# Kernel optimization log

Measured on AMD Instinct MI355X. Metric: run time of the kernel, lower is better.

## Reference

```python
import jax, jax.numpy as jnp
import numpy as np

B, C, H, W = 4, 64, 256, 256
HEADS = 4
HID = 128  # dim * ffn_expansion_factor
EPS = 1e-5


def _ln_chan(x, w, b):
    # LayerNorm over channel axis of [b,c,h,w] (equiv to to_3d -> LN over c -> to_4d)
    mu = x.mean(1, keepdims=True)
    var = jnp.mean((x - mu) ** 2, axis=1, keepdims=True)
    return (x - mu) / jnp.sqrt(var + EPS) * w[None, :, None, None] + b[None, :, None, None]


def _ln_last(x, w, b):
    mu = x.mean(-1, keepdims=True)
    var = jnp.mean((x - mu) ** 2, axis=-1, keepdims=True)
    return (x - mu) / jnp.sqrt(var + EPS) * w + b


def _conv1(x, Wt):
    # 1x1 conv, no bias; Wt: [out,in]
    return jnp.einsum('oi,bihw->bohw', Wt, x)


def _l2norm(x):
    # torch F.normalize(dim=-1): x / max(||x||, 1e-12)
    return x / jnp.maximum(jnp.linalg.norm(x, axis=-1, keepdims=True), 1e-12)


def _dct(inp1, inp2, Wq, Wk, Wv, temp):
    # Divide_Cross_Transformer: q from inp2, k/v from inp1; channel-wise attention
    b, c, h, w = inp1.shape
    ch = c // HEADS
    hw = h * w
    q = _conv1(inp2, Wq).reshape(b, HEADS, ch, hw)
    k = _conv1(inp1, Wk).reshape(b, HEADS, ch, hw)
    v = _conv1(inp1, Wv).reshape(b, HEADS, ch, hw)
    q = _l2norm(q)
    k = _l2norm(k)
    attn = jax.nn.softmax(jnp.einsum('bhcn,bhdn->bhcd', q, k) * temp[None], axis=-1)
    return attn, v  # attn: [b,head,ch,ch], v: [b,head,ch,hw]


def _ffn(x3, w1, b1, w2, b2):
    # torch nn.GELU default = exact erf
    hdn = jax.nn.gelu(jnp.einsum('bnc,hc->bnh', x3, w1) + b1, approximate=False)
    return jnp.einsum('bnh,ch->bnc', hdn, w2) + b2


def setup_inputs() -> dict:
    key = jax.random.key(0)
    ks = jax.random.split(key, 16)
    s = 0.05

    def n(k, shape):
        return jax.random.normal(k, shape, jnp.float32) * s

    ones = jnp.ones((C,), jnp.float32)
    zeros = jnp.zeros((C,), jnp.float32)
    return {
        'image': jax.random.normal(ks[0], (B, C, H, W), jnp.float32),
        'event': jax.random.normal(ks[1], (B, C, H, W), jnp.float32),
        'Wq_c': n(ks[2], (C, C)), 'Wk_c': n(ks[3], (C, C)), 'Wv_c': n(ks[4], (C, C)),
        'temp_c': jnp.ones((HEADS, 1, 1), jnp.float32),
        'Wq_d': n(ks[5], (C, C)), 'Wk_d': n(ks[6], (C, C)), 'Wv_d': n(ks[7], (C, C)),
        'temp_d': jnp.ones((HEADS, 1, 1), jnp.float32),
        'ln_img_w': ones, 'ln_img_b': zeros,
        'ln_evt_w': ones, 'ln_evt_b': zeros,
        'ln_com_w': ones, 'ln_com_b': zeros,
        'ln_dif_w': ones, 'ln_dif_b': zeros,
        'ln1_w': ones, 'ln1_b': zeros,
        'ln2_w': ones, 'ln2_b': zeros,
        'fc1c_w': n(ks[8], (HID, C)), 'fc1c_b': jnp.zeros((HID,), jnp.float32),
        'fc2c_w': n(ks[9], (C, HID)), 'fc2c_b': jnp.zeros((C,), jnp.float32),
        'fc1d_w': n(ks[10], (HID, C)), 'fc1d_b': jnp.zeros((HID,), jnp.float32),
        'fc2d_w': n(ks[11], (C, HID)), 'fc2d_b': jnp.zeros((C,), jnp.float32),
        'proj1_w': n(ks[12], (C, C)), 'proj2_w': n(ks[13], (C, C)),
    }


def reference(image, event, Wq_c, Wk_c, Wv_c, temp_c, Wq_d, Wk_d, Wv_d, temp_d,
              ln_img_w, ln_img_b, ln_evt_w, ln_evt_b, ln_com_w, ln_com_b,
              ln_dif_w, ln_dif_b, ln1_w, ln1_b, ln2_w, ln2_b,
              fc1c_w, fc1c_b, fc2c_w, fc2c_b, fc1d_w, fc1d_b, fc2d_w, fc2d_b,
              proj1_w, proj2_w):
    b, c, h, w = image.shape
    hw = h * w
    common = image + event
    differential = image - event

    ni = _ln_chan(image, ln_img_w, ln_img_b)
    ne = _ln_chan(event, ln_evt_w, ln_evt_b)
    nc = _ln_chan(common, ln_com_w, ln_com_b)
    nd = _ln_chan(differential, ln_dif_w, ln_dif_b)

    # common branch: shared conv weights (attn_common), attn maps multiplied
    a_ic, v_ic = _dct(ni, nc, Wq_c, Wk_c, Wv_c, temp_c)
    a_ec, v_ec = _dct(ne, nc, Wq_c, Wk_c, Wv_c, temp_c)
    a_c = a_ic * a_ec
    oc = jnp.einsum('bhcd,bhdn->bhcn', a_c, v_ic + v_ec)  # same attn for both matmuls
    oc = oc.reshape(b, c, h, w)
    oc = _conv1(oc, proj1_w)
    oc3 = oc.reshape(b, c, hw).transpose(0, 2, 1)  # b (hw) c
    oc3 = oc3 + _ffn(_ln_last(oc3, ln1_w, ln1_b), fc1c_w, fc1c_b, fc2c_w, fc2c_b)
    out_common = oc3.transpose(0, 2, 1).reshape(b, c, h, w)

    # differential branch: separate attn maps, not multiplied
    a_id, v_id = _dct(ni, nd, Wq_d, Wk_d, Wv_d, temp_d)
    a_ed, v_ed = _dct(ne, nd, Wq_d, Wk_d, Wv_d, temp_d)
    od = (jnp.einsum('bhcd,bhdn->bhcn', a_id, v_id)
          + jnp.einsum('bhcd,bhdn->bhcn', a_ed, v_ed))
    od = od.reshape(b, c, h, w)
    od = _conv1(od, proj2_w)
    od3 = od.reshape(b, c, hw).transpose(0, 2, 1)
    od3 = od3 + _ffn(_ln_last(od3, ln2_w, ln2_b), fc1d_w, fc1d_b, fc2d_w, fc2d_b)
    out_differential = od3.transpose(0, 2, 1).reshape(b, c, h, w)

    return (out_common, out_differential)
```

## Files before the change

kernel.cpp:

```cpp
#include <hip/hip_runtime.h>
#include <math.h>

typedef unsigned int u32;
typedef unsigned short u16;
typedef __attribute__((ext_vector_type(8))) short short8;
typedef __attribute__((ext_vector_type(4))) float float4v;

#define NBATCH 4
#define HW 65536

#define OFF_COV 0
#define OFF_T   131072
#define OFF_M   294912
#define OFF_P   344064
#define OFF_WC  393216
#define OFF_PAR 516096
#define WS_NEED ((size_t)(OFF_PAR + 1048576) * 4)

__device__ inline float bf2f(u16 h){ return __uint_as_float(((u32)h) << 16); }
__device__ inline u16 f2bf(float x){
  u32 u = __float_as_uint(x);
  u += 0x7fffu + ((u >> 16) & 1u);
  return (u16)(u >> 16);
}
__device__ inline u32 packbf2(float a, float b){
  u32 r;
  asm("v_cvt_pk_bf16_f32 %0, %1, %2" : "=v"(r) : "v"(a), "v"(b));
  return r;
}
__device__ inline float bfu(u32 u, int hi){
  return __uint_as_float(hi ? (u & 0xffff0000u) : (u << 16));
}

__device__ inline bool detect_f32(const void* probe, int t, int* s_cnt){
  if (t == 0) *s_cnt = 0;
  __syncthreads();
  u32 w = ((const u32*)probe)[t & 255];
  u32 ex = (w >> 7) & 0xffu;
  if (!(ex >= 113u && ex <= 133u)) atomicAdd(s_cnt, 1);
  __syncthreads();
  return *s_cnt >= 128;
}

__device__ inline bool detect_f32_512(const void* probe, int t, int* s_cnt){
  if (t == 0) *s_cnt = 0;
  __syncthreads();
  if (t < 256){
    u32 w = ((const u32*)probe)[t];
    u32 ex = (w >> 7) & 0xffu;
    if (!(ex >= 113u && ex <= 133u)) atomicAdd(s_cnt, 1);
  }
  __syncthreads();
  return *s_cnt >= 128;
}

__device__ inline void ld8(const u16* pb, const float* pf, size_t idx, bool f32, float* o){
  if (f32){
    const float4 a = *(const float4*)(pf + idx);
    const float4 b = *(const float4*)(pf + idx + 4);
    o[0]=a.x; o[1]=a.y; o[2]=a.z; o[3]=a.w; o[4]=b.x; o[5]=b.y; o[6]=b.z; o[7]=b.w;
  } else {
    uint4 r = *(const uint4*)(pb + idx);
    const u32* p = (const u32*)&r;
    #pragma unroll
    for (int j=0;j<8;j++) o[j] = bfu(p[j>>1], j&1);
  }
}

__device__ inline void softmax16(float* l){
  float m = l[0];
  #pragma unroll
  for (int i=1;i<16;i++) m = fmaxf(m, l[i]);
  float s = 0.f;
  #pragma unroll
  for (int i=0;i<16;i++){ l[i] = __expf(l[i]-m); s += l[i]; }
  float r = 1.0f/s;
  #pragma unroll
  for (int i=0;i<16;i++) l[i] *= r;
}

__global__ __launch_bounds__(256) void convert_all(
    const void* img,
    const void* t0, const void* t1, const void* t2, const void* t3,
    const void* t4, const void* t5, const void* t6, const void* t7,
    const void* t8, const void* t9, const void* t10, const void* t11,
    const void* t12, const void* t13, const void* t14, const void* t15,
    const void* t16, const void* t17, const void* t18, const void* t19,
    const void* t20, const void* t21, const void* t22, const void* t23,
    const void* t24, const void* t25, const void* t26, const void* t27,
    const void* t28, const void* t29,
    u16* __restrict__ wc)
{
  __shared__ int s_cnt;
  const int t = threadIdx.x;
  const bool f32 = detect_f32(img, t, &s_cnt);
  const int sizes[30] = {4096,4096,4096,4,4096,4096,4096,4,
                         64,64,64,64,64,64,64,64,64,64,64,64,
                         8192,128,8192,64,8192,128,8192,64,4096,4096};
  const void* srcs[30] = {t0,t1,t2,t3,t4,t5,t6,t7,t8,t9,t10,t11,t12,t13,t14,
                          t15,t16,t17,t18,t19,t20,t21,t22,t23,t24,t25,t26,t27,t28,t29};
  const int id = blockIdx.x;
  const void* s = srcs[id];
  const int n = sizes[id];
  u16* d = wc + (size_t)id*8192;
  for (int j = t; j < n; j += 256)
    d[j] = f32 ? f2bf(((const float*)s)[j]) : ((const u16*)s)[j];
}

__global__ __launch_bounds__(512, 4) void k1_cov(
    const void* __restrict__ img, const void* __restrict__ evt,
    const u16* __restrict__ lniw, const u16* __restrict__ lnib,
    const u16* __restrict__ lnew, const u16* __restrict__ lneb,
    const u16* __restrict__ lncw, const u16* __restrict__ lncb,
    const u16* __restrict__ lndw, const u16* __restrict__ lndb,
    float* __restrict__ cov, float* __restrict__ par, int use_par)
{
  __shared__ u16 NtL[4*64*72];
  __shared__ float spart[8][64][5];
  __shared__ float params[8][64];
  __shared__ int s_cnt;

  const int t = threadIdx.x;
  const bool f32 = detect_f32_512(img, t, &s_cnt);
  const u16* imgb = (const u16*)img; const float* imgf = (const float*)img;
  const u16* evtb = (const u16*)evt; const float* evtf = (const float*)evt;

  const int b = blockIdx.x >> 7;
  const int P0 = (blockIdx.x & 127) * 512;
  const int ch = t >> 3, pg = t & 7;
  const int wave = t >> 6, lane = t & 63, l15 = lane & 15, quad = lane >> 4;

  float wi=bf2f(lniw[ch]), bi=bf2f(lnib[ch]);
  float we=bf2f(lnew[ch]), be=bf2f(lneb[ch]);
  float wc_=bf2f(lncw[ch]), bc_=bf2f(lncb[ch]);
  float wd_=bf2f(lndw[ch]), bd_=bf2f(lndb[ch]);

  const int va = (wave==3)?0 : (wave==7)?1 : (wave<3)?2:3;
  const int vb = (wave==0)?2 : (wave==4)?3 :
                 ((wave==2)||(wave==6)||(wave==7))?1:0;

  float4v acc[4][4];
  #pragma unroll
  for (int i=0;i<4;i++)
    #pragma unroll
    for (int j=0;j<4;j++) acc[i][j]=(float4v)0.f;

  const size_t base = (size_t)(b*64 + ch) * HW;

  for (int it = 0; it < 8; ++it){
    const int p0 = P0 + it*64;
    float A[8], B[8];
    ld8(imgb, imgf, base + p0 + pg*8, f32, A);
    ld8(evtb, evtf, base + p0 + pg*8, f32, B);

    #pragma unroll 1
    for (int jp=0;jp<4;jp++){
// ... 233 lines not shown

__global__ __launch_bounds__(256) void p2c(
    const u16* __restrict__ proj1, const u16* __restrict__ proj2,
    float* __restrict__ ws)
{
  __shared__ float WL[64][65];
  __shared__ float CL[64][64];
  const int t = threadIdx.x;
  const int b = blockIdx.x & 3;
  const int which = blockIdx.x >> 2;
  const u16* W = (which==0)? proj1 : proj2;
  const float* Cm = ws + OFF_M + ((size_t)which*NBATCH + b)*4096;
  { int r = t>>2, c0 = (t&3)*16;
    #pragma unroll
    for (int i=0;i<16;i++) WL[r][c0+i] = bf2f(W[r*64 + c0 + i]);
    const float4* s = (const float4*)(Cm + r*64 + c0);
    float4* d = (float4*)&CL[r][c0];
    d[0]=s[0]; d[1]=s[1]; d[2]=s[2]; d[3]=s[3]; }
  __syncthreads();
  const int r = t>>2, k0 = (t&3)*16;
  float a[16];
  #pragma unroll
  for (int i=0;i<16;i++) a[i]=0.f;
  for (int m=0;m<64;m++){
    float wv = WL[r][m];
    #pragma unroll
    for (int i=0;i<16;i++) a[i] = fmaf(wv, CL[m][k0+i], a[i]);
  }
  float* o = ws + OFF_P + ((size_t)which*NBATCH + b)*4096 + r*64 + k0;
  #pragma unroll
  for (int i=0;i<16;i++) o[i] = a[i];
}

__global__ __launch_bounds__(256) void k3_common(
    const void* __restrict__ img, const void* __restrict__ evt,
    const u16* __restrict__ lniw, const u16* __restrict__ lnib,
    const u16* __restrict__ lnew, const u16* __restrict__ lneb,
    const u16* __restrict__ ln1w, const u16* __restrict__ ln1b,
    const u16* __restrict__ fc1w, const u16* __restrict__ fc1b,
    const u16* __restrict__ fc2w, const u16* __restrict__ fc2b,
    const float* __restrict__ Pmat, void* __restrict__ outp, size_t obase,
    const float* __restrict__ par, int use_par)
{
  __shared__ u16 fc1L[128*72];
  __shared__ u16 fc2L[64*136];
  __shared__ u16 PcL[64*72];
  __shared__ u16 SB[64*136];
  __shared__ float spart[4][64][4];
  __shared__ float params[64][4];
  __shared__ float b1L[128];
  __shared__ float b2L[64];
  __shared__ int s_cnt;

  const int t = threadIdx.x;
  const bool f32 = detect_f32(img, t, &s_cnt);
  const u16* imgb = (const u16*)img; const float* imgf = (const float*)img;
  const u16* evtb = (const u16*)evt; const float* evtf = (const float*)evt;

  const int b = blockIdx.x >> 8;
  const int P0 = (blockIdx.x & 255) * 256;
  const int chg = t >> 3, pg = t & 7, ch0 = chg*2;
  const int wave = t >> 6, lane = t & 63, l15 = lane & 15, quad = lane >> 4;

  { int row = t >> 1, c0 = (t & 1)*32;
    const uint4* s = (const uint4*)(fc1w + row*64 + c0);
    uint4* d = (uint4*)&fc1L[row*72 + c0];
    d[0]=s[0]; d[1]=s[1]; d[2]=s[2]; d[3]=s[3]; }
  { int row = t >> 2, c0 = (t & 3)*32;
    const uint4* s = (const uint4*)(fc2w + row*128 + c0);
    uint4* d = (uint4*)&fc2L[row*136 + c0];
    d[0]=s[0]; d[1]=s[1]; d[2]=s[2]; d[3]=s[3]; }
  { int row = t >> 2, c0 = (t & 3)*16;
    const float* s = Pmat + (size_t)b*4096 + row*64 + c0;
    u32 u[8];
    #pragma unroll
    for (int i=0;i<8;i++) u[i] = packbf2(s[2*i], s[2*i+1]);
    uint4* d = (uint4*)&PcL[row*72 + c0];
    d[0] = make_uint4(u[0],u[1],u[2],u[3]);
    d[1] = make_uint4(u[4],u[5],u[6],u[7]); }
  if (t < 128) b1L[t] = bf2f(fc1b[t]);
  if (t < 64)  b2L[t] = bf2f(fc2b[t]);

  float wi0=bf2f(lniw[ch0]), wi1=bf2f(lniw[ch0+1]);
  float we0=bf2f(lnew[ch0]), we1=bf2f(lnew[ch0+1]);
  float bs0=bf2f(lnib[ch0]) + bf2f(lneb[ch0]);
  float bs1=bf2f(lnib[ch0+1]) + bf2f(lneb[ch0+1]);
  float w1r[4], b1r[4];
  #pragma unroll
  for (int nj=0;nj<4;nj++){ w1r[nj]=bf2f(ln1w[nj*16+l15]); b1r[nj]=bf2f(ln1b[nj*16+l15]); }
  __syncthreads();

  const size_t base_i = (size_t)(b*64 + ch0)*HW;
  for (int it=0; it<4; ++it){
    const int p0 = P0 + it*64;
    float A0[8], A1[8], B0[8], B1[8];
    ld8(imgb, imgf, base_i + p0 + pg*8, f32, A0);
    ld8(imgb, imgf, base_i + HW + p0 + pg*8, f32, A1);
    ld8(evtb, evtf, base_i + p0 + pg*8, f32, B0);
    ld8(evtb, evtf, base_i + HW + p0 + pg*8, f32, B1);

    if (use_par){
      const float4* pp = (const float4*)(par + ((size_t)b*HW + p0 + pg*8)*4);
      #pragma unroll
      for (int j=0;j<8;j++){
        float4 pr = pp[j];
        float a0=(A0[j]-pr.x)*pr.y, a1=(A1[j]-pr.x)*pr.y;
        float c0f=(B0[j]-pr.z)*pr.w, c1f=(B1[j]-pr.z)*pr.w;
        float n0 = fmaf(a0, wi0, fmaf(c0f, we0, bs0));
        float n1 = fmaf(a1, wi1, fmaf(c1f, we1, bs1));
        *(u32*)&SB[(pg*8+j)*136 + ch0] = packbf2(n0, n1);
      }
    } else {
      float si[8], sii[8], se[8], see[8];
      #pragma unroll
      for (int j=0;j<8;j++){
        float xi0=A0[j], xi1=A1[j], xe0=B0[j], xe1=B1[j];
        si[j]=xi0+xi1; sii[j]=fmaf(xi0,xi0,xi1*xi1);
        se[j]=xe0+xe1; see[j]=fmaf(xe0,xe0,xe1*xe1);
      }
      #pragma unroll
      for (int m=8;m<=32;m<<=1)
        #pragma unroll
        for (int j=0;j<8;j++){
          si[j]+=__shfl_xor(si[j],m); sii[j]+=__shfl_xor(sii[j],m);
          se[j]+=__shfl_xor(se[j],m); see[j]+=__shfl_xor(see[j],m);
        }
      if ((chg&7)==0){
        #pragma unroll
        for (int j=0;j<8;j++){
          spart[wave][pg*8+j][0]=si[j]; spart[wave][pg*8+j][1]=sii[j];
          spart[wave][pg*8+j][2]=se[j]; spart[wave][pg*8+j][3]=see[j];
        }
      }
      __syncthreads();
      if (t<64){
        float S0=0,S1=0,S2=0,S3=0;
        #pragma unroll
        for (int w=0;w<4;w++){ S0+=spart[w][t][0]; S1+=spart[w][t][1]; S2+=spart[w][t][2]; S3+=spart[w][t][3]; }
        const float inv=0.015625f;
        float mu_i=S0*inv, mu_e=S2*inv;
        float r_i=rsqrtf(fmaf(S1,inv,-mu_i*mu_i)+1e-5f);
        float r_e=rsqrtf(fmaf(S3,inv,-mu_e*mu_e)+1e-5f);
        params[t][0]=mu_i; params[t][1]=r_i; params[t][2]=mu_e; params[t][3]=r_e;
      }
      __syncthreads();
      #pragma unroll
      for (int j=0;j<8;j++){
        float4 pr = *(const float4*)&params[pg*8+j][0];
        float a0=(A0[j]-pr.x)*pr.y, a1=(A1[j]-pr.x)*pr.y;
        float c0f=(B0[j]-pr.z)*pr.w, c1f=(B1[j]-pr.z)*pr.w;
        float n0 = fmaf(a0, wi0, fmaf(c0f, we0, bs0));
        float n1 = fmaf(a1, wi1, fmaf(c1f, we1, bs1));
        *(u32*)&SB[(pg*8+j)*136 + ch0] = packbf2(n0, n1);
      }
    }
    __syncthreads();
    float4v acc1[4];
    #pragma unroll
    for (int nj=0;nj<4;nj++) acc1[nj]=(float4v)0.f;
    const int px_row = wave*16 + l15;
    #pragma unroll
    for (int ks=0;ks<2;ks++){
      const int off = ks*32 + quad*8;
      short8 af = *(const short8*)&SB[px_row*136 + off];
      #pragma unroll
      for (int nj=0;nj<4;nj++){
        short8 bw = *(const short8*)&PcL[(nj*16+l15)*72 + off];
        acc1[nj] = __builtin_amdgcn_mfma_f32_16x16x32_bf16(af, bw, acc1[nj], 0,0,0);
      }
    }
    float s[4], sq[4];
    #pragma unroll
    for (int j=0;j<4;j++){
      s[j] = acc1[0][j]+acc1[1][j]+acc1[2][j]+acc1[3][j];
      sq[j] = acc1[0][j]*acc1[0][j];
      sq[j] = fmaf(acc1[1][j],acc1[1][j],sq[j]);
      sq[j] = fmaf(acc1[2][j],acc1[2][j],sq[j]);
      sq[j] = fmaf(acc1[3][j],acc1[3][j],sq[j]);
    }
    #pragma unroll
    for (int m=1;m<=8;m<<=1)
      #pragma unroll
      for (int j=0;j<4;j++){ s[j]+=__shfl_xor(s[j],m); sq[j]+=__shfl_xor(sq[j],m); }
    float muj[4], rj[4];
    #pragma unroll
    for (int j=0;j<4;j++){
      muj[j]=s[j]*0.015625f;
// ... 31 lines not shown
      }
    }
    float4v accO[4];
    #pragma unroll
    for (int nj=0;nj<4;nj++) accO[nj]=(float4v)0.f;
    #pragma unroll
    for (int ks=0;ks<4;ks++){
      const int off = ks*32+quad*8;
      short8 ag = *(const short8*)&SB[px_row*136 + off];
      #pragma unroll
      for (int nj=0;nj<4;nj++){
        short8 bw = *(const short8*)&fc2L[(nj*16+l15)*136 + off];
        accO[nj] = __builtin_amdgcn_mfma_f32_16x16x32_bf16(ag, bw, accO[nj], 0,0,0);
      }
    }
    const int px0 = p0 + wave*16 + quad*4;
    #pragma unroll
    for (int nj=0;nj<4;nj++){
      float bb = b2L[nj*16+l15];
      int r = nj*16+l15;
      float v0 = acc1[nj][0] + accO[nj][0] + bb;
      float v1 = acc1[nj][1] + accO[nj][1] + bb;
      float v2 = acc1[nj][2] + accO[nj][2] + bb;
      float v3 = acc1[nj][3] + accO[nj][3] + bb;
      size_t oi = obase + (size_t)(b*64 + r)*HW + px0;
      if (f32){ float4 fv; fv.x=v0; fv.y=v1; fv.z=v2; fv.w=v3;
        *(float4*)((float*)outp + oi) = fv; }
      else *(uint2*)((u16*)outp + oi) = make_uint2(packbf2(v0,v1), packbf2(v2,v3));
    }
    __syncthreads();
  }
}

__global__ __launch_bounds__(256) void k3_diff(
    const void* __restrict__ img, const void* __restrict__ evt,
    const u16* __restrict__ lniw, const u16* __restrict__ lnib,
    const u16* __restrict__ lnew, const u16* __restrict__ lneb,
    const u16* __restrict__ ln2w, const u16* __restrict__ ln2b,
    const u16* __restrict__ fc1w, const u16* __restrict__ fc1b,
    const u16* __restrict__ fc2w, const u16* __restrict__ fc2b,
    const float* __restrict__ Pmat, void* __restrict__ outp, size_t obase,
    const float* __restrict__ par, int use_par)
{
  __shared__ u16 fc1L[128*72];
  __shared__ u16 fc2L[64*136];
  __shared__ u16 PiL[64*72];
  __shared__ u16 PeL[64*72];
  __shared__ u16 N2L[64*144];
  __shared__ float spart[4][64][4];
  __shared__ float params[64][4];
  __shared__ float b1L[128];
  __shared__ float b2L[64];
  __shared__ int s_cnt;

  const int t = threadIdx.x;
  const bool f32 = detect_f32(img, t, &s_cnt);
  const u16* imgb = (const u16*)img; const float* imgf = (const float*)img;
  const u16* evtb = (const u16*)evt; const float* evtf = (const float*)evt;

  const int b = blockIdx.x >> 8;
  const int P0 = (blockIdx.x & 255) * 256;
  const int chg = t >> 3, pg = t & 7, ch0 = chg*2;
  const int wave = t >> 6, lane = t & 63, l15 = lane & 15, quad = lane >> 4;

  { int row = t >> 1, c0 = (t & 1)*32;
    const uint4* s = (const uint4*)(fc1w + row*64 + c0);
    uint4* d = (uint4*)&fc1L[row*72 + c0];
    d[0]=s[0]; d[1]=s[1]; d[2]=s[2]; d[3]=s[3]; }
  { int row = t >> 2, c0 = (t & 3)*32;
    const uint4* s = (const uint4*)(fc2w + row*128 + c0);
    uint4* d = (uint4*)&fc2L[row*136 + c0];
    d[0]=s[0]; d[1]=s[1]; d[2]=s[2]; d[3]=s[3]; }
  { int row = t >> 2, c0 = (t & 3)*16;
    const float* si_ = Pmat + ((size_t)1*NBATCH + b)*4096 + row*64 + c0;
    const float* se_ = Pmat + ((size_t)2*NBATCH + b)*4096 + row*64 + c0;
    u32 u[8];
    #pragma unroll
    for (int i=0;i<8;i++) u[i] = packbf2(si_[2*i], si_[2*i+1]);
    uint4* d = (uint4*)&PiL[row*72 + c0];
    d[0] = make_uint4(u[0],u[1],u[2],u[3]); d[1] = make_uint4(u[4],u[5],u[6],u[7]);
    #pragma unroll
    for (int i=0;i<8;i++) u[i] = packbf2(se_[2*i], se_[2*i+1]);
    uint4* d2 = (uint4*)&PeL[row*72 + c0];
    d2[0] = make_uint4(u[0],u[1],u[2],u[3]); d2[1] = make_uint4(u[4],u[5],u[6],u[7]); }
  if (t < 128) b1L[t] = bf2f(fc1b[t]);
  if (t < 64)  b2L[t] = bf2f(fc2b[t]);

  float wi0=bf2f(lniw[ch0]), wi1=bf2f(lniw[ch0+1]);
  float bi0=bf2f(lnib[ch0]), bi1=bf2f(lnib[ch0+1]);
  float we0=bf2f(lnew[ch0]), we1=bf2f(lnew[ch0+1]);
  float be0=bf2f(lneb[ch0]), be1=bf2f(lneb[ch0+1]);
  float w1r[4], b1r[4];
  #pragma unroll
  for (int nj=0;nj<4;nj++){ w1r[nj]=bf2f(ln2w[nj*16+l15]); b1r[nj]=bf2f(ln2b[nj*16+l15]); }
  __syncthreads();

  const size_t base_i = (size_t)(b*64 + ch0)*HW;
  for (int it=0; it<4; ++it){
    const int p0 = P0 + it*64;
    float A0[8], A1[8], B0[8], B1[8];
    ld8(imgb, imgf, base_i + p0 + pg*8, f32, A0);
    ld8(imgb, imgf, base_i + HW + p0 + pg*8, f32, A1);
    ld8(evtb, evtf, base_i + p0 + pg*8, f32, B0);
    ld8(evtb, evtf, base_i + HW + p0 + pg*8, f32, B1);

    if (use_par){
      const float4* pp = (const float4*)(par + ((size_t)b*HW + p0 + pg*8)*4);
      #pragma unroll
      for (int j=0;j<8;j++){
        float4 pr = pp[j];
        float a0=(A0[j]-pr.x)*pr.y, a1=(A1[j]-pr.x)*pr.y;
        float c0f=(B0[j]-pr.z)*pr.w, c1f=(B1[j]-pr.z)*pr.w;
        *(u32*)&N2L[(pg*8+j)*144 + ch0]      = packbf2(fmaf(a0,wi0,bi0), fmaf(a1,wi1,bi1));
        *(u32*)&N2L[(pg*8+j)*144 + 72 + ch0] = packbf2(fmaf(c0f,we0,be0), fmaf(c1f,we1,be1));
      }
    } else {
      float si[8], sii[8], se[8], see[8];
      #pragma unroll
      for (int j=0;j<8;j++){
        float xi0=A0[j], xi1=A1[j], xe0=B0[j], xe1=B1[j];
        si[j]=xi0+xi1; sii[j]=fmaf(xi0,xi0,xi1*xi1);
        se[j]=xe0+xe1; see[j]=fmaf(xe0,xe0,xe1*xe1);
      }
      #pragma unroll
      for (int m=8;m<=32;m<<=1)
        #pragma unroll
        for (int j=0;j<8;j++){
          si[j]+=__shfl_xor(si[j],m); sii[j]+=__shfl_xor(sii[j],m);
          se[j]+=__shfl_xor(se[j],m); see[j]+=__shfl_xor(see[j],m);
        }
      if ((chg&7)==0){
        #pragma unroll
        for (int j=0;j<8;j++){
          spart[wave][pg*8+j][0]=si[j]; spart[wave][pg*8+j][1]=sii[j];
          spart[wave][pg*8+j][2]=se[j]; spart[wave][pg*8+j][3]=see[j];
        }
      }
      __syncthreads();
      if (t<64){
        float S0=0,S1=0,S2=0,S3=0;
        #pragma unroll
        for (int w=0;w<4;w++){ S0+=spart[w][t][0]; S1+=spart[w][t][1]; S2+=spart[w][t][2]; S3+=spart[w][t][3]; }
        const float inv=0.015625f;
        float mu_i=S0*inv, mu_e=S2*inv;
        float r_i=rsqrtf(fmaf(S1,inv,-mu_i*mu_i)+1e-5f);
        float r_e=rsqrtf(fmaf(S3,inv,-mu_e*mu_e)+1e-5f);
        params[t][0]=mu_i; params[t][1]=r_i; params[t][2]=mu_e; params[t][3]=r_e;
      }
      __syncthreads();
      #pragma unroll
      for (int j=0;j<8;j++){
        float4 pr = *(const float4*)&params[pg*8+j][0];
        float a0=(A0[j]-pr.x)*pr.y, a1=(A1[j]-pr.x)*pr.y;
        float c0f=(B0[j]-pr.z)*pr.w, c1f=(B1[j]-pr.z)*pr.w;
        *(u32*)&N2L[(pg*8+j)*144 + ch0]      = packbf2(fmaf(a0,wi0,bi0), fmaf(a1,wi1,bi1));
        *(u32*)&N2L[(pg*8+j)*144 + 72 + ch0] = packbf2(fmaf(c0f,we0,be0), fmaf(c1f,we1,be1));
      }
    }
    __syncthreads();
    float4v acc1[4];
    #pragma unroll
    for (int nj=0;nj<4;nj++) acc1[nj]=(float4v)0.f;
    const int px_row = wave*16 + l15;
    #pragma unroll
    for (int ks=0;ks<2;ks++){
      const int off = ks*32 + quad*8;
      short8 ai = *(const short8*)&N2L[px_row*144 + off];
      short8 ae = *(const short8*)&N2L[px_row*144 + 72 + off];
      #pragma unroll
      for (int nj=0;nj<4;nj++){
        short8 bwi = *(const short8*)&PiL[(nj*16+l15)*72 + off];
        acc1[nj] = __builtin_amdgcn_mfma_f32_16x16x32_bf16(ai, bwi, acc1[nj], 0,0,0);
        short8 bwe = *(const short8*)&PeL[(nj*16+l15)*72 + off];
        acc1[nj] = __builtin_amdgcn_mfma_f32_16x16x32_bf16(ae, bwe, acc1[nj], 0,0,0);
      }
    }
    float s[4], sq[4];
    #pragma unroll
    for (int j=0;j<4;j++){
      s[j] = acc1[0][j]+acc1[1][j]+acc1[2][j]+acc1[3][j];
      sq[j] = acc1[0][j]*acc1[0][j];
      sq[j] = fmaf(acc1[1][j],acc1[1][j],sq[j]);
      sq[j] = fmaf(acc1[2][j],acc1[2][j],sq[j]);
      sq[j] = fmaf(acc1[3][j],acc1[3][j],sq[j]);
    }
    #pragma unroll
    for (int m=1;m<=8;m<<=1)
      #pragma unroll
      for (int j=0;j<4;j++){ s[j]+=__shfl_xor(s[j],m); sq[j]+=__shfl_xor(sq[j],m); }
    float muj[4], rj[4];
// ... 59 lines not shown
      if (f32){ float4 fv; fv.x=v0; fv.y=v1; fv.z=v2; fv.w=v3;
        *(float4*)((float*)outp + oi) = fv; }
      else *(uint2*)((u16*)outp + oi) = make_uint2(packbf2(v0,v1), packbf2(v2,v3));
    }
    __syncthreads();
  }
}

extern "C" void kernel_launch(void* const* d_in, const int* in_sizes, int n_in,
                              void* d_out, int out_size, void* d_ws, size_t ws_size,
                              hipStream_t stream)
{
  const void* img = d_in[0];
  const void* evt = d_in[1];
  float* ws = (float*)d_ws;
  u16* wc = (u16*)(ws + OFF_WC);
  float* par = ws + OFF_PAR;
  const int use_par = (ws_size >= WS_NEED) ? 1 : 0;
  #define SLOT(i) (wc + (size_t)((i)-2)*8192)

  hipMemsetAsync(ws, 0, 131072*sizeof(float), stream);
  convert_all<<<dim3(30), dim3(256), 0, stream>>>(img,
      d_in[2], d_in[3], d_in[4], d_in[5], d_in[6], d_in[7], d_in[8], d_in[9],
      d_in[10], d_in[11], d_in[12], d_in[13], d_in[14], d_in[15], d_in[16], d_in[17],
      d_in[18], d_in[19], d_in[20], d_in[21], d_in[22], d_in[23], d_in[24], d_in[25],
      d_in[26], d_in[27], d_in[28], d_in[29], d_in[30], d_in[31], wc);
  k1_cov<<<dim3(512), dim3(512), 0, stream>>>(img, evt,
      SLOT(10), SLOT(11), SLOT(12), SLOT(13), SLOT(14), SLOT(15), SLOT(16), SLOT(17),
      ws, par, use_par);
  p2a<<<dim3(40), dim3(256), 0, stream>>>(SLOT(2), SLOT(3), SLOT(6), SLOT(7), ws);
  p2b<<<dim3(4), dim3(256), 0, stream>>>(ws, SLOT(2), SLOT(3), SLOT(6), SLOT(7),
      SLOT(4), SLOT(8), SLOT(5), SLOT(9));
  p2c<<<dim3(12), dim3(256), 0, stream>>>(SLOT(30), SLOT(31), ws);
  k3_common<<<dim3(1024), dim3(256), 0, stream>>>(img, evt,
      SLOT(10), SLOT(11), SLOT(12), SLOT(13), SLOT(18), SLOT(19),
      SLOT(22), SLOT(23), SLOT(24), SLOT(25), ws + OFF_P, d_out, (size_t)0, par, use_par);
  k3_diff<<<dim3(1024), dim3(256), 0, stream>>>(img, evt,
      SLOT(10), SLOT(11), SLOT(12), SLOT(13), SLOT(20), SLOT(21),
      SLOT(26), SLOT(27), SLOT(28), SLOT(29), ws + OFF_P, d_out, (size_t)16777216, par, use_par);
  #undef SLOT
}
```

Measured before the change: 567.9 us.

## Add larger-block k3 kernels specialized for precomputed LayerNorm params

Adds k3_common_hi (512 threads, 512 pixels per block) and k3_diff_hi (1024 threads, 1024 pixels per block) that always read the precomputed per-pixel LN parameters. They are dispatched when the workspace is large enough, and the original kernels keep only the in-kernel statistics path. The aim is to spread the weight and projection staging into LDS over more pixels per block and to remove the runtime branch. The cost is much larger LDS per block, especially the 256x144 buffer in the diff kernel, which can lower occupancy. Unused ld8_issue/ld8_unpack helpers are also added.

```diff
diff --git a/kernel.cpp b/kernel.cpp
--- a/kernel.cpp
+++ b/kernel.cpp
@@ -42,7 +42,7 @@
   return *s_cnt >= 128;
 }
 
-__device__ inline bool detect_f32_512(const void* probe, int t, int* s_cnt){
+__device__ inline bool detect_f32_wide(const void* probe, int t, int* s_cnt){
   if (t == 0) *s_cnt = 0;
   __syncthreads();
   if (t < 256){
@@ -62,6 +62,26 @@
   } else {
     uint4 r = *(const uint4*)(pb + idx);
     const u32* p = (const u32*)&r;
+    #pragma unroll
+    for (int j=0;j<8;j++) o[j] = bfu(p[j>>1], j&1);
+  }
+}
+
+__device__ inline void ld8_issue(const u16* pb, const float* pf, size_t idx, bool f32, uint4* r2){
+  if (f32){
+    r2[0] = *(const uint4*)(pf + idx);
+    r2[1] = *(const uint4*)(pf + idx + 4);
+  } else {
+    r2[0] = *(const uint4*)(pb + idx);
+  }
+}
+__device__ inline void ld8_unpack(const uint4* r2, bool f32, float* o){
+  if (f32){
+    const float* q = (const float*)r2;
+    #pragma unroll
+    for (int j=0;j<8;j++) o[j] = q[j];
+  } else {
+    const u32* p = (const u32*)r2;
     #pragma unroll
     for (int j=0;j<8;j++) o[j] = bfu(p[j>>1], j&1);
   }
@@ -121,7 +141,7 @@
   __shared__ int s_cnt;
 
   const int t = threadIdx.x;
-  const bool f32 = detect_f32_512(img, t, &s_cnt);
+  const bool f32 = detect_f32_wide(img, t, &s_cnt);
   const u16* imgb = (const u16*)img; const float* imgf = (const float*)img;
   const u16* evtb = (const u16*)evt; const float* evtf = (const float*)evt;
 
@@ -421,7 +441,7 @@
   for (int i=0;i<16;i++) o[i] = a[i];
 }
 
-__global__ __launch_bounds__(256) void k3_common(
+__global__ __launch_bounds__(512, 4) void k3_common_hi(
     const void* __restrict__ img, const void* __restrict__ evt,
     const u16* __restrict__ lniw, const u16* __restrict__ lnib,
     const u16* __restrict__ lnew, const u16* __restrict__ lneb,
@@ -429,7 +449,361 @@
     const u16* __restrict__ fc1w, const u16* __restrict__ fc1b,
     const u16* __restrict__ fc2w, const u16* __restrict__ fc2b,
     const float* __restrict__ Pmat, void* __restrict__ outp, size_t obase,
-    const float* __restrict__ par, int use_par)
+    const float* __restrict__ par)
+{
+  __shared__ u16 fc1L[128*72];
+  __shared__ u16 fc2L[64*136];
+  __shared__ u16 PcL[64*72];
+  __shared__ u16 SB[128*136];
+  __shared__ float b1L[128];
+  __shared__ float b2L[64];
+  __shared__ int s_cnt;
+
+  const int t = threadIdx.x;
+  const bool f32 = detect_f32_wide(img, t, &s_cnt);
+  const u16* imgb = (const u16*)img; const float* imgf = (const float*)img;
+  const u16* evtb = (const u16*)evt; const float* evtf = (const float*)evt;
+
+  const int b = blockIdx.x >> 7;
+  const int P0 = (blockIdx.x & 127) * 512;
+  const int pg = t & 15, ch0 = (t >> 4) * 2;
+  const int wave = t >> 6, lane = t & 63, l15 = lane & 15, quad = lane >> 4;
+
+  if (t < 256){
+    { int row = t >> 1, c0 = (t & 1)*32;
+      const uint4* s = (const uint4*)(fc1w + row*64 + c0);
+      uint4* d = (uint4*)&fc1L[row*72 + c0];
+      d[0]=s[0]; d[1]=s[1]; d[2]=s[2]; d[3]=s[3]; }
+    { int row = t >> 2, c0 = (t & 3)*32;
+      const uint4* s = (const uint4*)(fc2w + row*128 + c0);
+      uint4* d = (uint4*)&fc2L[row*136 + c0];
+      d[0]=s[0]; d[1]=s[1]; d[2]=s[2]; d[3]=s[3]; }
+    { int row = t >> 2, c0 = (t & 3)*16;
+      const float* s = Pmat + (size_t)b*4096 + row*64 + c0;
+      u32 u[8];
+      #pragma unroll
+      for (int i=0;i<8;i++) u[i] = packbf2(s[2*i], s[2*i+1]);
+      uint4* d = (uint4*)&PcL[row*72 + c0];
+      d[0] = make_uint4(u[0],u[1],u[2],u[3]);
+      d[1] = make_uint4(u[4],u[5],u[6],u[7]); }
+  }
+  if (t < 128) b1L[t] = bf2f(fc1b[t]);
+  if (t < 64)  b2L[t] = bf2f(fc2b[t]);
+
+  float wi0=bf2f(lniw[ch0]), wi1=bf2f(lniw[ch0+1]);
+  float we0=bf2f(lnew[ch0]), we1=bf2f(lnew[ch0+1]);
+  float bs0=bf2f(lnib[ch0]) + bf2f(lneb[ch0]);
+  float bs1=bf2f(lnib[ch0+1]) + bf2f(lneb[ch0+1]);
+  float w1r[4], b1r[4];
+  #pragma unroll
+  for (int nj=0;nj<4;nj++){ w1r[nj]=bf2f(ln1w[nj*16+l15]); b1r[nj]=bf2f(ln1b[nj*16+l15]); }
+  __syncthreads();
+
+  const size_t base_i = (size_t)(b*64 + ch0)*HW;
+  for (int it=0; it<4; ++it){
+    const int p0 = P0 + it*128;
+    float A0[8], A1[8], B0[8], B1[8];
+    ld8(imgb, imgf, base_i + p0 + pg*8, f32, A0);
+    ld8(imgb, imgf, base_i + HW + p0 + pg*8, f32, A1);
+    ld8(evtb, evtf, base_i + p0 + pg*8, f32, B0);
+    ld8(evtb, evtf, base_i + HW + p0 + pg*8, f32, B1);
+    {
+      const float4* pp = (const float4*)(par + ((size_t)b*HW + p0 + pg*8)*4);
+      #pragma unroll
+      for (int j=0;j<8;j++){
+        float4 pr = pp[j];
+        float a0=(A0[j]-pr.x)*pr.y, a1=(A1[j]-pr.x)*pr.y;
+        float c0f=(B0[j]-pr.z)*pr.w, c1f=(B1[j]-pr.z)*pr.w;
+        float n0 = fmaf(a0, wi0, fmaf(c0f, we0, bs0));
+        float n1 = fmaf(a1, wi1, fmaf(c1f, we1, bs1));
+        *(u32*)&SB[(pg*8+j)*136 + ch0] = packbf2(n0, n1);
+      }
+    }
+    __syncthreads();
+    float4v acc1[4];
+    #pragma unroll
+    for (int nj=0;nj<4;nj++) acc1[nj]=(float4v)0.f;
+    const int px_row = wave*16 + l15;
+    #pragma unroll
+    for (int ks=0;ks<2;ks++){
+      const int off = ks*32 + quad*8;
+      short8 af = *(const short8*)&SB[px_row*136 + off];
+      #pragma unroll
+      for (int nj=0;nj<4;nj++){
+        short8 bw = *(const short8*)&PcL[(nj*16+l15)*72 + off];
+        acc1[nj] = __builtin_amdgcn_mfma_f32_16x16x32_bf16(af, bw, acc1[nj], 0,0,0);
+      }
+    }
+    float s[4], sq[4];
+    #pragma unroll
+    for (int j=0;j<4;j++){
+      s[j] = acc1[0][j]+acc1[1][j]+acc1[2][j]+acc1[3][j];
+      sq[j] = acc1[0][j]*acc1[0][j];
+      sq[j] = fmaf(acc1[1][j],acc1[1][j],sq[j]);
+      sq[j] = fmaf(acc1[2][j],acc1[2][j],sq[j]);
+      sq[j] = fmaf(acc1[3][j],acc1[3][j],sq[j]);
+    }
+    #pragma unroll
+    for (int m=1;m<=8;m<<=1)
+      #pragma unroll
+      for (int j=0;j<4;j++){ s[j]+=__shfl_xor(s[j],m); sq[j]+=__shfl_xor(sq[j],m); }
+    float muj[4], rj[4];
+    #pragma unroll
+    for (int j=0;j<4;j++){
+      muj[j]=s[j]*0.015625f;
+      rj[j]=rsqrtf(fmaf(sq[j],0.015625f,-muj[j]*muj[j])+1e-5f);
+    }
+    #pragma unroll
+    for (int nj=0;nj<4;nj++)
+      #pragma unroll
+      for (int j=0;j<4;j++){
+        float tv = (acc1[nj][j]-muj[j])*rj[j];
+        tv = fmaf(tv, w1r[nj], b1r[nj]);
+        SB[(wave*16+quad*4+j)*136 + nj*16+l15] = f2bf(tv);
+      }
+    float4v accF[8];
+    #pragma unroll
+    for (int nh=0;nh<8;nh++) accF[nh]=(float4v)0.f;
+    #pragma unroll
+    for (int ks=0;ks<2;ks++){
+      const int off = ks*32+quad*8;
+      short8 af = *(const short8*)&SB[px_row*136 + off];
+      #pragma unroll
+      for (int nh=0;nh<8;nh++){
+        short8 bw = *(const short8*)&fc1L[(nh*16+l15)*72 + off];
+        accF[nh] = __builtin_amdgcn_mfma_f32_16x16x32_bf16(af, bw, accF[nh], 0,0,0);
+      }
+    }
+    #pragma unroll
+    for (int nh=0;nh<8;nh++){
+      float bb = b1L[nh*16+l15];
+      #pragma unroll
+      for (int j=0;j<4;j++){
+        float v = accF[nh][j] + bb;
+        float g = 0.5f*v*(1.0f + erff(v*0.70710678118654752f));
+        SB[(wave*16+quad*4+j)*136 + nh*16+l15] = f2bf(g);
+      }
+    }
+    float4v accO[4];
+    #pragma unroll
+    for (int nj=0;nj<4;nj++) accO[nj]=(float4v)0.f;
+    #pragma unroll
+    for (int ks=0;ks<4;ks++){
+      const int off = ks*32+quad*8;
+      short8 ag = *(const short8*)&SB[px_row*136 + off];
+      #pragma unroll
+      for (int nj=0;nj<4;nj++){
+        short8 bw = *(const short8*)&fc2L[(nj*16+l15)*136 + off];
+        accO[nj] = __builtin_amdgcn_mfma_f32_16x16x32_bf16(ag, bw, accO[nj], 0,0,0);
+      }
+    }
+    const int px0 = p0 + wave*16 + quad*4;
+    #pragma unroll
+    for (int nj=0;nj<4;nj++){
+      float bb = b2L[nj*16+l15];
+      int r = nj*16+l15;
+      float v0 = acc1[nj][0] + accO[nj][0] + bb;
+      float v1 = acc1[nj][1] + accO[nj][1] + bb;
+      float v2 = acc1[nj][2] + accO[nj][2] + bb;
+      float v3 = acc1[nj][3] + accO[nj][3] + bb;
+      size_t oi = obase + (size_t)(b*64 + r)*HW + px0;
+      if (f32){ float4 fv; fv.x=v0; fv.y=v1; fv.z=v2; fv.w=v3;
+        *(float4*)((float*)outp + oi) = fv; }
+      else *(uint2*)((u16*)outp + oi) = make_uint2(packbf2(v0,v1), packbf2(v2,v3));
+    }
+    __syncthreads();
+  }
+}
+
+__global__ __launch_bounds__(1024) void k3_diff_hi(
+    const void* __restrict__ img, const void* __restrict__ evt,
+    const u16* __restrict__ lniw, const u16* __restrict__ lnib,
+    const u16* __restrict__ lnew, const u16* __restrict__ lneb,
+    const u16* __restrict__ ln2w, const u16* __restrict__ ln2b,
+    const u16* __restrict__ fc1w, const u16* __restrict__ fc1b,
+    const u16* __restrict__ fc2w, const u16* __restrict__ fc2b,
+    const float* __restrict__ Pmat, void* __restrict__ outp, size_t obase,
+    const float* __restrict__ par)
+{
+  __shared__ u16 fc1L[128*72];
+  __shared__ u16 fc2L[64*136];
+  __shared__ u16 PiL[64*72];
+  __shared__ u16 PeL[64*72];
+  __shared__ u16 N2L[256*144];
+  __shared__ float b1L[128];
+  __shared__ float b2L[64];
+  __shared__ int s_cnt;
+
+  const int t = threadIdx.x;
+  const bool f32 = detect_f32_wide(img, t, &s_cnt);
+  const u16* imgb = (const u16*)img; const float* imgf = (const float*)img;
+  const u16* evtb = (const u16*)evt; const float* evtf = (const float*)evt;
+
+  const int b = blockIdx.x >> 6;
+  const int P0 = (blockIdx.x & 63) * 1024;
+  const int pg = t & 31, ch0 = (t >> 5) * 2;
+  const int wave = t >> 6, lane = t & 63, l15 = lane & 15, quad = lane >> 4;
+
+  if (t < 256){
+    { int row = t >> 1, c0 = (t & 1)*32;
+      const uint4* s = (const uint4*)(fc1w + row*64 + c0);
+      uint4* d = (uint4*)&fc1L[row*72 + c0];
+      d[0]=s[0]; d[1]=s[1]; d[2]=s[2]; d[3]=s[3]; }
+    { int row = t >> 2, c0 = (t & 3)*32;
+      const uint4* s = (const uint4*)(fc2w + row*128 + c0);
+      uint4* d = (uint4*)&fc2L[row*136 + c0];
+      d[0]=s[0]; d[1]=s[1]; d[2]=s[2]; d[3]=s[3]; }
+    { int row = t >> 2, c0 = (t & 3)*16;
+      const float* si_ = Pmat + ((size_t)1*NBATCH + b)*4096 + row*64 + c0;
+      const float* se_ = Pmat + ((size_t)2*NBATCH + b)*4096 + row*64 + c0;
+      u32 u[8];
+      #pragma unroll
+      for (int i=0;i<8;i++) u[i] = packbf2(si_[2*i], si_[2*i+1]);
+      uint4* d = (uint4*)&PiL[row*72 + c0];
+      d[0] = make_uint4(u[0],u[1],u[2],u[3]); d[1] = make_uint4(u[4],u[5],u[6],u[7]);
+      #pragma unroll
+      for (int i=0;i<8;i++) u[i] = packbf2(se_[2*i], se_[2*i+1]);
+      uint4* d2 = (uint4*)&PeL[row*72 + c0];
+      d2[0] = make_uint4(u[0],u[1],u[2],u[3]); d2[1] = make_uint4(u[4],u[5],u[6],u[7]); }
+  }
+  if (t < 128) b1L[t] = bf2f(fc1b[t]);
+  if (t < 64)  b2L[t] = bf2f(fc2b[t]);
+
+  float wi0=bf2f(lniw[ch0]), wi1=bf2f(lniw[ch0+1]);
+  float bi0=bf2f(lnib[ch0]), bi1=bf2f(lnib[ch0+1]);
+  float we0=bf2f(lnew[ch0]), we1=bf2f(lnew[ch0+1]);
+  float be0=bf2f(lneb[ch0]), be1=bf2f(lneb[ch0+1]);
+  float w1r[4], b1r[4];
+  #pragma unroll
+  for (int nj=0;nj<4;nj++){ w1r[nj]=bf2f(ln2w[nj*16+l15]); b1r[nj]=bf2f(ln2b[nj*16+l15]); }
+  __syncthreads();
+
+  const size_t base_i = (size_t)(b*64 + ch0)*HW;
+  for (int it=0; it<4; ++it){
+    const int p0 = P0 + it*256;
+    float A0[8], A1[8], B0[8], B1[8];
+    ld8(imgb, imgf, base_i + p0 + pg*8, f32, A0);
+    ld8(imgb, imgf, base_i + HW + p0 + pg*8, f32, A1);
+    ld8(evtb, evtf, base_i + p0 + pg*8, f32, B0);
+    ld8(evtb, evtf, base_i + HW + p0 + pg*8, f32, B1);
+    {
+      const float4* pp = (const float4*)(par + ((size_t)b*HW + p0 + pg*8)*4);
+      #pragma unroll
+      for (int j=0;j<8;j++){
+        float4 pr = pp[j];
+        float a0=(A0[j]-pr.x)*pr.y, a1=(A1[j]-pr.x)*pr.y;
+        float c0f=(B0[j]-pr.z)*pr.w, c1f=(B1[j]-pr.z)*pr.w;
+        *(u32*)&N2L[(pg*8+j)*144 + ch0]      = packbf2(fmaf(a0,wi0,bi0), fmaf(a1,wi1,bi1));
+        *(u32*)&N2L[(pg*8+j)*144 + 72 + ch0] = packbf2(fmaf(c0f,we0,be0), fmaf(c1f,we1,be1));
+      }
+    }
+    __syncthreads();
+    float4v acc1[4];
+    #pragma unroll
+    for (int nj=0;nj<4;nj++) acc1[nj]=(float4v)0.f;
+    const int px_row = wave*16 + l15;
+    #pragma unroll
+    for (int ks=0;ks<2;ks++){
+      const int off = ks*32 + quad*8;
+      short8 ai = *(const short8*)&N2L[px_row*144 + off];
+      short8 ae = *(const short8*)&N2L[px_row*144 + 72 + off];
+      #pragma unroll
+      for (int nj=0;nj<4;nj++){
+        short8 bwi = *(const short8*)&PiL[(nj*16+l15)*72 + off];
+        acc1[nj] = __builtin_amdgcn_mfma_f32_16x16x32_bf16(ai, bwi, acc1[nj], 0,0,0);
+        short8 bwe = *(const short8*)&PeL[(nj*16+l15)*72 + off];
+        acc1[nj] = __builtin_amdgcn_mfma_f32_16x16x32_bf16(ae, bwe, acc1[nj], 0,0,0);
+      }
+    }
+    float s[4], sq[4];
+    #pragma unroll
+    for (int j=0;j<4;j++){
+      s[j] = acc1[0][j]+acc1[1][j]+acc1[2][j]+acc1[3][j];
+      sq[j] = acc1[0][j]*acc1[0][j];
+      sq[j] = fmaf(acc1[1][j],acc1[1][j],sq[j]);
+      sq[j] = fmaf(acc1[2][j],acc1[2][j],sq[j]);
+      sq[j] = fmaf(acc1[3][j],acc1[3][j],sq[j]);
+    }
+    #pragma unroll
+    for (int m=1;m<=8;m<<=1)
+      #pragma unroll
+      for (int j=0;j<4;j++){ s[j]+=__shfl_xor(s[j],m); sq[j]+=__shfl_xor(sq[j],m); }
+    float muj[4], rj[4];
+    #pragma unroll
+    for (int j=0;j<4;j++){
+      muj[j]=s[j]*0.015625f;
+      rj[j]=rsqrtf(fmaf(sq[j],0.015625f,-muj[j]*muj[j])+1e-5f);
+    }
+    #pragma unroll
+    for (int nj=0;nj<4;nj++)
+      #pragma unroll
+      for (int j=0;j<4;j++){
+        float tv = (acc1[nj][j]-muj[j])*rj[j];
+        tv = fmaf(tv, w1r[nj], b1r[nj]);
+        N2L[(wave*16+quad*4+j)*144 + nj*16+l15] = f2bf(tv);
+      }
+    float4v accF[8];
+    #pragma unroll
+    for (int nh=0;nh<8;nh++) accF[nh]=(float4v)0.f;
+    #pragma unroll
+    for (int ks=0;ks<2;ks++){
+      const int off = ks*32+quad*8;
+      short8 af = *(const short8*)&N2L[px_row*144 + off];
+      #pragma unroll
+      for (int nh=0;nh<8;nh++){
+        short8 bw = *(const short8*)&fc1L[(nh*16+l15)*72 + off];
+        accF[nh] = __builtin_amdgcn_mfma_f32_16x16x32_bf16(af, bw, accF[nh], 0,0,0);
+      }
+    }
+    #pragma unroll
+    for (int nh=0;nh<8;nh++){
+      float bb = b1L[nh*16+l15];
+      #pragma unroll
+      for (int j=0;j<4;j++){
+        float v = accF[nh][j] + bb;
+        float g = 0.5f*v*(1.0f + erff(v*0.70710678118654752f));
+        N2L[(wave*16+quad*4+j)*144 + nh*16+l15] = f2bf(g);
+      }
+    }
+    float4v accO[4];
+    #pragma unroll
+    for (int nj=0;nj<4;nj++) accO[nj]=(float4v)0.f;
+    #pragma unroll
+    for (int ks=0;ks<4;ks++){
+      const int off = ks*32+quad*8;
+      short8 ag = *(const short8*)&N2L[px_row*144 + off];
+      #pragma unroll
+      for (int nj=0;nj<4;nj++){
+        short8 bw = *(const short8*)&fc2L[(nj*16+l15)*136 + off];
+        accO[nj] = __builtin_amdgcn_mfma_f32_16x16x32_bf16(ag, bw, accO[nj], 0,0,0);
+      }
+    }
+    const int px0 = p0 + wave*16 + quad*4;
+    #pragma unroll
+    for (int nj=0;nj<4;nj++){
+      float bb = b2L[nj*16+l15];
+      int r = nj*16+l15;
+      float v0 = acc1[nj][0] + accO[nj][0] + bb;
+      float v1 = acc1[nj][1] + accO[nj][1] + bb;
+      float v2 = acc1[nj][2] + accO[nj][2] + bb;
+      float v3 = acc1[nj][3] + accO[nj][3] + bb;
+      size_t oi = obase + (size_t)(b*64 + r)*HW + px0;
+      if (f32){ float4 fv; fv.x=v0; fv.y=v1; fv.z=v2; fv.w=v3;
+        *(float4*)((float*)outp + oi) = fv; }
+      else *(uint2*)((u16*)outp + oi) = make_uint2(packbf2(v0,v1), packbf2(v2,v3));
+    }
+    __syncthreads();
+  }
+}
+
+__global__ __launch_bounds__(256, 2) void k3_common(
+    const void* __restrict__ img, const void* __restrict__ evt,
+    const u16* __restrict__ lniw, const u16* __restrict__ lnib,
+    const u16* __restrict__ lnew, const u16* __restrict__ lneb,
+    const u16* __restrict__ ln1w, const u16* __restrict__ ln1b,
+    const u16* __restrict__ fc1w, const u16* __restrict__ fc1b,
+    const u16* __restrict__ fc2w, const u16* __restrict__ fc2b,
+    const float* __restrict__ Pmat, void* __restrict__ outp, size_t obase)
 {
   __shared__ u16 fc1L[128*72];
   __shared__ u16 fc2L[64*136];
@@ -488,60 +862,47 @@
     ld8(evtb, evtf, base_i + p0 + pg*8, f32, B0);
     ld8(evtb, evtf, base_i + HW + p0 + pg*8, f32, B1);
 
-    if (use_par){
-      const float4* pp = (const float4*)(par + ((size_t)b*HW + p0 + pg*8)*4);
+    float si[8], sii[8], se[8], see[8];
+    #pragma unroll
+    for (int j=0;j<8;j++){
+      float xi0=A0[j], xi1=A1[j], xe0=B0[j], xe1=B1[j];
+      si[j]=xi0+xi1; sii[j]=fmaf(xi0,xi0,xi1*xi1);
+      se[j]=xe0+xe1; see[j]=fmaf(xe0,xe0,xe1*xe1);
+    }
+    #pragma unroll
+    for (int m=8;m<=32;m<<=1)
       #pragma unroll
       for (int j=0;j<8;j++){
-        float4 pr = pp[j];
-        float a0=(A0[j]-pr.x)*pr.y, a1=(A1[j]-pr.x)*pr.y;
-        float c0f=(B0[j]-pr.z)*pr.w, c1f=(B1[j]-pr.z)*pr.w;
-        float n0 = fmaf(a0, wi0, fmaf(c0f, we0, bs0));
-        float n1 = fmaf(a1, wi1, fmaf(c1f, we1, bs1));
-        *(u32*)&SB[(pg*8+j)*136 + ch0] = packbf2(n0, n1);
-      }
-    } else {
-      float si[8], sii[8], se[8], see[8];
+        si[j]+=__shfl_xor(si[j],m); sii[j]+=__shfl_xor(sii[j],m);
+        se[j]+=__shfl_xor(se[j],m); see[j]+=__shfl_xor(see[j],m);
+      }
+    if ((chg&7)==0){
       #pragma unroll
       for (int j=0;j<8;j++){
-        float xi0=A0[j], xi1=A1[j], xe0=B0[j], xe1=B1[j];
-        si[j]=xi0+xi1; sii[j]=fmaf(xi0,xi0,xi1*xi1);
-        se[j]=xe0+xe1; see[j]=fmaf(xe0,xe0,xe1*xe1);
-      }
-      #pragma unroll
-      for (int m=8;m<=32;m<<=1)
-        #pragma unroll
-        for (int j=0;j<8;j++){
-          si[j]+=__shfl_xor(si[j],m); sii[j]+=__shfl_xor(sii[j],m);
-          se[j]+=__shfl_xor(se[j],m); see[j]+=__shfl_xor(see[j],m);
-        }
-      if ((chg&7)==0){
-        #pragma unroll
-        for (int j=0;j<8;j++){
-          spart[wave][pg*8+j][0]=si[j]; spart[wave][pg*8+j][1]=sii[j];
-          spart[wave][pg*8+j][2]=se[j]; spart[wave][pg*8+j][3]=see[j];
-        }
-      }
-      __syncthreads();
-      if (t<64){
-        float S0=0,S1=0,S2=0,S3=0;
-        #pragma unroll
-        for (int w=0;w<4;w++){ S0+=spart[w][t][0]; S1+=spart[w][t][1]; S2+=spart[w][t][2]; S3+=spart[w][t][3]; }
-        const float inv=0.015625f;
-        float mu_i=S0*inv, mu_e=S2*inv;
-        float r_i=rsqrtf(fmaf(S1,inv,-mu_i*mu_i)+1e-5f);
-        float r_e=rsqrtf(fmaf(S3,inv,-mu_e*mu_e)+1e-5f);
-        params[t][0]=mu_i; params[t][1]=r_i; params[t][2]=mu_e; params[t][3]=r_e;
-      }
-      __syncthreads();
-      #pragma unroll
-      for (int j=0;j<8;j++){
-        float4 pr = *(const float4*)&params[pg*8+j][0];
-        float a0=(A0[j]-pr.x)*pr.y, a1=(A1[j]-pr.x)*pr.y;
-        float c0f=(B0[j]-pr.z)*pr.w, c1f=(B1[j]-pr.z)*pr.w;
-        float n0 = fmaf(a0, wi0, fmaf(c0f, we0, bs0));
-        float n1 = fmaf(a1, wi1, fmaf(c1f, we1, bs1));
-        *(u32*)&SB[(pg*8+j)*136 + ch0] = packbf2(n0, n1);
-      }
+        spart[wave][pg*8+j][0]=si[j]; spart[wave][pg*8+j][1]=sii[j];
+        spart[wave][pg*8+j][2]=se[j]; spart[wave][pg*8+j][3]=see[j];
+      }
+    }
+    __syncthreads();
+    if (t<64){
+      float S0=0,S1=0,S2=0,S3=0;
+      #pragma unroll
+      for (int w=0;w<4;w++){ S0+=spart[w][t][0]; S1+=spart[w][t][1]; S2+=spart[w][t][2]; S3+=spart[w][t][3]; }
+      const float inv=0.015625f;
+      float mu_i=S0*inv, mu_e=S2*inv;
+      float r_i=rsqrtf(fmaf(S1,inv,-mu_i*mu_i)+1e-5f);
+      float r_e=rsqrtf(fmaf(S3,inv,-mu_e*mu_e)+1e-5f);
+      params[t][0]=mu_i; params[t][1]=r_i; params[t][2]=mu_e; params[t][3]=r_e;
+    }
+    __syncthreads();
+    #pragma unroll
+    for (int j=0;j<8;j++){
+      float4 pr = *(const float4*)&params[pg*8+j][0];
+      float a0=(A0[j]-pr.x)*pr.y, a1=(A1[j]-pr.x)*pr.y;
+      float c0f=(B0[j]-pr.z)*pr.w, c1f=(B1[j]-pr.z)*pr.w;
+      float n0 = fmaf(a0, wi0, fmaf(c0f, we0, bs0));
+      float n1 = fmaf(a1, wi1, fmaf(c1f, we1, bs1));
+      *(u32*)&SB[(pg*8+j)*136 + ch0] = packbf2(n0, n1);
     }
     __syncthreads();
     float4v acc1[4];
@@ -639,15 +1000,14 @@
   }
 }
 
-__global__ __launch_bounds__(256) void k3_diff(
+__global__ __launch_bounds__(256, 2) void k3_diff(
     const void* __restrict__ img, const void* __restrict__ evt,
     const u16* __restrict__ lniw, const u16* __restrict__ lnib,
     const u16* __restrict__ lnew, const u16* __restrict__ lneb,
     const u16* __restrict__ ln2w, const u16* __restrict__ ln2b,
     const u16* __restrict__ fc1w, const u16* __restrict__ fc1b,
     const u16* __restrict__ fc2w, const u16* __restrict__ fc2b,
-    const float* __restrict__ Pmat, void* __restrict__ outp, size_t obase,
-    const float* __restrict__ par, int use_par)
+    const float* __restrict__ Pmat, void* __restrict__ outp, size_t obase)
 {
   __shared__ u16 fc1L[128*72];
   __shared__ u16 fc2L[64*136];
@@ -711,58 +1071,46 @@
     ld8(evtb, evtf, base_i + p0 + pg*8, f32, B0);
     ld8(evtb, evtf, base_i + HW + p0 + pg*8, f32, B1);
 
-    if (use_par){
-      const float4* pp = (const float4*)(par + ((size_t)b*HW + p0 + pg*8)*4);
+    float si[8], sii[8], se[8], see[8];
+    #pragma unroll
+    for (int j=0;j<8;j++){
+      float xi0=A0[j], xi1=A1[j], xe0=B0[j], xe1=B1[j];
+      si[j]=xi0+xi1; sii[j]=fmaf(xi0,xi0,xi1*xi1);
+      se[j]=xe0+xe1; see[j]=fmaf(xe0,xe0,xe1*xe1);
+    }
+    #pragma unroll
+    for (int m=8;m<=32;m<<=1)
       #pragma unroll
       for (int j=0;j<8;j++){
-        float4 pr = pp[j];
-        float a0=(A0[j]-pr.x)*pr.y, a1=(A1[j]-pr.x)*pr.y;
-        float c0f=(B0[j]-pr.z)*pr.w, c1f=(B1[j]-pr.z)*pr.w;
-        *(u32*)&N2L[(pg*8+j)*144 + ch0]      = packbf2(fmaf(a0,wi0,bi0), fmaf(a1,wi1,bi1));
-        *(u32*)&N2L[(pg*8+j)*144 + 72 + ch0] = packbf2(fmaf(c0f,we0,be0), fmaf(c1f,we1,be1));
-      }
-    } else {
-      float si[8], sii[8], se[8], see[8];
+        si[j]+=__shfl_xor(si[j],m); sii[j]+=__shfl_xor(sii[j],m);
+        se[j]+=__shfl_xor(se[j],m); see[j]+=__shfl_xor(see[j],m);
+      }
+    if ((chg&7)==0){
       #pragma unroll
       for (int j=0;j<8;j++){
-        float xi0=A0[j], xi1=A1[j], xe0=B0[j], xe1=B1[j];
-        si[j]=xi0+xi1; sii[j]=fmaf(xi0,xi0,xi1*xi1);
-        se[j]=xe0+xe1; see[j]=fmaf(xe0,xe0,xe1*xe1);
-      }
-      #pragma unroll
-      for (int m=8;m<=32;m<<=1)
-        #pragma unroll
-        for (int j=0;j<8;j++){
-          si[j]+=__shfl_xor(si[j],m); sii[j]+=__shfl_xor(sii[j],m);
-          se[j]+=__shfl_xor(se[j],m); see[j]+=__shfl_xor(see[j],m);
-        }
-      if ((chg&7)==0){
-        #pragma unroll
-        for (int j=0;j<8;j++){
-          spart[wave][pg*8+j][0]=si[j]; spart[wave][pg*8+j][1]=sii[j];
-          spart[wave][pg*8+j][2]=se[j]; spart[wave][pg*8+j][3]=see[j];
-        }
-      }
-      __syncthreads();
-      if (t<64){
-        float S0=0,S1=0,S2=0,S3=0;
-        #pragma unroll
-        for (int w=0;w<4;w++){ S0+=spart[w][t][0]; S1+=spart[w][t][1]; S2+=spart[w][t][2]; S3+=spart[w][t][3]; }
-        const float inv=0.015625f;
-        float mu_i=S0*inv, mu_e=S2*inv;
-        float r_i=rsqrtf(fmaf(S1,inv,-mu_i*mu_i)+1e-5f);
-        float r_e=rsqrtf(fmaf(S3,inv,-mu_e*mu_e)+1e-5f);
-        params[t][0]=mu_i; params[t][1]=r_i; params[t][2]=mu_e; params[t][3]=r_e;
-      }
-      __syncthreads();
-      #pragma unroll
-      for (int j=0;j<8;j++){
-        float4 pr = *(const float4*)&params[pg*8+j][0];
-        float a0=(A0[j]-pr.x)*pr.y, a1=(A1[j]-pr.x)*pr.y;
-        float c0f=(B0[j]-pr.z)*pr.w, c1f=(B1[j]-pr.z)*pr.w;
-        *(u32*)&N2L[(pg*8+j)*144 + ch0]      = packbf2(fmaf(a0,wi0,bi0), fmaf(a1,wi1,bi1));
-        *(u32*)&N2L[(pg*8+j)*144 + 72 + ch0] = packbf2(fmaf(c0f,we0,be0), fmaf(c1f,we1,be1));
-      }
+        spart[wave][pg*8+j][0]=si[j]; spart[wave][pg*8+j][1]=sii[j];
+        spart[wave][pg*8+j][2]=se[j]; spart[wave][pg*8+j][3]=see[j];
+      }
+    }
+    __syncthreads();
+    if (t<64){
+      float S0=0,S1=0,S2=0,S3=0;
+      #pragma unroll
+      for (int w=0;w<4;w++){ S0+=spart[w][t][0]; S1+=spart[w][t][1]; S2+=spart[w][t][2]; S3+=spart[w][t][3]; }
+      const float inv=0.015625f;
+      float mu_i=S0*inv, mu_e=S2*inv;
+      float r_i=rsqrtf(fmaf(S1,inv,-mu_i*mu_i)+1e-5f);
+      float r_e=rsqrtf(fmaf(S3,inv,-mu_e*mu_e)+1e-5f);
+      params[t][0]=mu_i; params[t][1]=r_i; params[t][2]=mu_e; params[t][3]=r_e;
+    }
+    __syncthreads();
+    #pragma unroll
+    for (int j=0;j<8;j++){
+      float4 pr = *(const float4*)&params[pg*8+j][0];
+      float a0=(A0[j]-pr.x)*pr.y, a1=(A1[j]-pr.x)*pr.y;
+      float c0f=(B0[j]-pr.z)*pr.w, c1f=(B1[j]-pr.z)*pr.w;
+      *(u32*)&N2L[(pg*8+j)*144 + ch0]      = packbf2(fmaf(a0,wi0,bi0), fmaf(a1,wi1,bi1));
+      *(u32*)&N2L[(pg*8+j)*144 + 72 + ch0] = packbf2(fmaf(c0f,we0,be0), fmaf(c1f,we1,be1));
     }
     __syncthreads();
     float4v acc1[4];
@@ -888,11 +1236,20 @@
   p2b<<<dim3(4), dim3(256), 0, stream>>>(ws, SLOT(2), SLOT(3), SLOT(6), SLOT(7),
       SLOT(4), SLOT(8), SLOT(5), SLOT(9));
   p2c<<<dim3(12), dim3(256), 0, stream>>>(SLOT(30), SLOT(31), ws);
-  k3_common<<<dim3(1024), dim3(256), 0, stream>>>(img, evt,
-      SLOT(10), SLOT(11), SLOT(12), SLOT(13), SLOT(18), SLOT(19),
-      SLOT(22), SLOT(23), SLOT(24), SLOT(25), ws + OFF_P, d_out, (size_t)0, par, use_par);
-  k3_diff<<<dim3(1024), dim3(256), 0, stream>>>(img, evt,
-      SLOT(10), SLOT(11), SLOT(12), SLOT(13), SLOT(20), SLOT(21),
-      SLOT(26), SLOT(27), SLOT(28), SLOT(29), ws + OFF_P, d_out, (size_t)16777216, par, use_par);
+  if (use_par){
+    k3_common_hi<<<dim3(512), dim3(512), 0, stream>>>(img, evt,
+        SLOT(10), SLOT(11), SLOT(12), SLOT(13), SLOT(18), SLOT(19),
+        SLOT(22), SLOT(23), SLOT(24), SLOT(25), ws + OFF_P, d_out, (size_t)0, par);
+    k3_diff_hi<<<dim3(256), dim3(1024), 0, stream>>>(img, evt,
+        SLOT(10), SLOT(11), SLOT(12), SLOT(13), SLOT(20), SLOT(21),
+        SLOT(26), SLOT(27), SLOT(28), SLOT(29), ws + OFF_P, d_out, (size_t)16777216, par);
+  } else {
+    k3_common<<<dim3(1024), dim3(256), 0, stream>>>(img, evt,
+        SLOT(10), SLOT(11), SLOT(12), SLOT(13), SLOT(18), SLOT(19),
+        SLOT(22), SLOT(23), SLOT(24), SLOT(25), ws + OFF_P, d_out, (size_t)0);
+    k3_diff<<<dim3(1024), dim3(256), 0, stream>>>(img, evt,
+        SLOT(10), SLOT(11), SLOT(12), SLOT(13), SLOT(20), SLOT(21),
+        SLOT(26), SLOT(27), SLOT(28), SLOT(29), ws + OFF_P, d_out, (size_t)16777216);
+  }
   #undef SLOT
 }
```

Result: no change. 578.9 us (+1.9%).
